# Optimization experiments

Hardware: AMD Instinct MI355X
Metric: run time of the kernel (lower is better)

## Reference

```python
import jax, jax.numpy as jnp
import numpy as np

N = 100000      # nodes
E = 1600000     # edges (avg degree 16)
IN_C = 128
OUT_C = 64
HID = 2 * OUT_C  # 128


def setup_inputs() -> dict:
    key = jax.random.key(0)
    ks = jax.random.split(key, 8)
    x = jax.random.normal(ks[0], (N, IN_C), dtype=jnp.float32)
    edge_index = jax.random.randint(ks[1], (2, E), 0, N, dtype=jnp.int32)
    # Glorot-ish init for GCN weight matrices, zero bias (PyG default)
    w1 = jax.random.normal(ks[2], (IN_C, HID), dtype=jnp.float32) / np.sqrt(IN_C)
    b1 = jnp.zeros((HID,), jnp.float32)
    w_mu = jax.random.normal(ks[3], (HID, OUT_C), dtype=jnp.float32) / np.sqrt(HID)
    b_mu = jnp.zeros((OUT_C,), jnp.float32)
    w_ls = jax.random.normal(ks[4], (HID, OUT_C), dtype=jnp.float32) / np.sqrt(HID)
    b_ls = jnp.zeros((OUT_C,), jnp.float32)
    return {"x": x, "edge_index": edge_index, "w1": w1, "b1": b1,
            "w_mu": w_mu, "b_mu": b_mu, "w_ls": w_ls, "b_ls": b_ls}


def _gcn_conv(h, w, b, src, dst, norm, n):
    # linear transform, then normalized sparse aggregation src -> dst
    h = h @ w                                   # [N, out]
    msg = h[src] * norm[:, None]                # [E+N, out] gather
    out = jax.ops.segment_sum(msg, dst, num_segments=n)  # scatter-add
    return out + b


def reference(x, edge_index, w1, b1, w_mu, b_mu, w_ls, b_ls):
    n = x.shape[0]
    # GCN normalization with self-loops (edge_weight=None -> all ones)
    loops = jnp.arange(n, dtype=edge_index.dtype)
    src = jnp.concatenate([edge_index[0], loops])
    dst = jnp.concatenate([edge_index[1], loops])
    ew = jnp.ones(src.shape[0], dtype=x.dtype)
    deg = jax.ops.segment_sum(ew, dst, num_segments=n)
    dinv = jnp.where(deg > 0, jax.lax.rsqrt(jnp.maximum(deg, 1e-12)), 0.0)
    norm = dinv[src] * ew * dinv[dst]           # D^-1/2 A_hat D^-1/2

    h = jax.nn.relu(_gcn_conv(x, w1, b1, src, dst, norm, n))
    mu = _gcn_conv(h, w_mu, b_mu, src, dst, norm, n)
    logstd = _gcn_conv(h, w_ls, b_ls, src, dst, norm, n)
    return (mu, logstd)
```

## Files before the change

kernel.cpp:

```cpp
#include <hip/hip_runtime.h>
#include <hip/hip_bf16.h>

#define CH 128
#define OC 64
#define NBINS 1024
#define NCHK  256
#define BSH   7

typedef __attribute__((ext_vector_type(4))) float f32x4;
typedef __attribute__((ext_vector_type(8))) float f32x8;
typedef __attribute__((ext_vector_type(8))) short bf16x8;
typedef __attribute__((ext_vector_type(8))) ushort u16x8;

static __device__ __forceinline__ float bf2f(ushort u) {
  return __uint_as_float(((unsigned)u) << 16);
}
static __device__ __forceinline__ ushort f2bf(float f) {
  __hip_bfloat16 h = __float2bfloat16(f);
  return *reinterpret_cast<ushort*>(&h);
}
static __device__ __forceinline__ void fma8(float w, u16x8 v, f32x8& a) {
#pragma unroll
  for (int j = 0; j < 8; j++) a[j] = fmaf(w, bf2f((ushort)v[j]), a[j]);
}

__global__ void k_pre(const float* __restrict__ x, ushort* __restrict__ y, int nx,
                      const float* __restrict__ w1, const float* __restrict__ wmu,
                      const float* __restrict__ wls, const float* __restrict__ bmu,
                      const float* __restrict__ bls, ushort* __restrict__ Wt0,
                      ushort* __restrict__ Wt1, float* __restrict__ bc) {
  int gid = blockIdx.x * 256 + threadIdx.x;
  int i = gid * 4;
  if (i < nx) {
    float4 v = *(const float4*)&x[i];
    ushort4 o; o.x = f2bf(v.x); o.y = f2bf(v.y); o.z = f2bf(v.z); o.w = f2bf(v.w);
    *(ushort4*)&y[i] = o;
  }
  if (gid < 16384) {
    int c = gid >> 7, k = gid & 127;
    Wt0[c * 128 + k] = f2bf(w1[k * 128 + c]);
    float v = (c < 64) ? wmu[k * 64 + c] : wls[k * 64 + (c - 64)];
    Wt1[c * 128 + k] = f2bf(v);
    if (gid < 128) bc[gid] = (gid < 64) ? bmu[gid] : bls[gid - 64];
  }
}


__global__ __launch_bounds__(256) void k_s1(const int* __restrict__ dst,
                                            int* __restrict__ bcnt, int ne, int cs) {
  __shared__ int h[NBINS];
  for (int j = threadIdx.x; j < NBINS; j += 256) h[j] = 0;
  __syncthreads();
  int e0 = blockIdx.x * cs, e1 = min(e0 + cs, ne);
  for (int e = e0 + threadIdx.x; e < e1; e += 256)
    atomicAdd(&h[dst[e] >> BSH], 1);
  __syncthreads();
  for (int j = threadIdx.x; j < NBINS; j += 256)
    bcnt[blockIdx.x * NBINS + j] = h[j];
}

__global__ __launch_bounds__(256) void k_s2a(const int* __restrict__ bcnt,
                                             int* __restrict__ curT,
                                             int* __restrict__ total) {
  __shared__ int s[NCHK];
  int b = blockIdx.x, t = threadIdx.x;
  int v = bcnt[t * NBINS + b];
  s[t] = v; __syncthreads();
  for (int off = 1; off < NCHK; off <<= 1) {
    int u = (t >= off) ? s[t - off] : 0;
    __syncthreads();
    s[t] += u;
    __syncthreads();
  }
  curT[b * NCHK + t] = s[t] - v;
  if (t == NCHK - 1) total[b] = s[t];
}

__global__ void k_s2b(const int* __restrict__ total, int* __restrict__ base) {
  __shared__ int s[256];
  int t = threadIdx.x;
  int loc[4]; int sum = 0;
#pragma unroll
  for (int j = 0; j < 4; j++) { loc[j] = total[t * 4 + j]; sum += loc[j]; }
  s[t] = sum; __syncthreads();
  int own = sum;
  for (int off = 1; off < 256; off <<= 1) {
    int u = (t >= off) ? s[t - off] : 0;
    __syncthreads();
    s[t] += u;
    __syncthreads();
  }
  int excl = s[t] - own;
#pragma unroll
  for (int j = 0; j < 4; j++) { base[t * 4 + j] = excl; excl += loc[j]; }
  if (t == 255) base[NBINS] = excl;
}

__global__ __launch_bounds__(256) void k_s3(const int* __restrict__ src,
    const int* __restrict__ dst, const int* __restrict__ curT,
    const int* __restrict__ base, unsigned* __restrict__ rec, int ne, int cs) {
  __shared__ int lcur[NBINS];
  int blk = blockIdx.x;
  for (int b = threadIdx.x; b < NBINS; b += 256)
    lcur[b] = curT[b * NCHK + blk] + base[b];
  __syncthreads();
  int e0 = blk * cs, e1 = min(e0 + cs, ne);
  for (int e = e0 + threadIdx.x; e < e1; e += 256) {
    int d = dst[e], sv = src[e];
    int pos = atomicAdd(&lcur[d >> BSH], 1);
    rec[pos] = ((unsigned)sv << BSH) | (unsigned)(d & 127);
  }
}

__global__ __launch_bounds__(256) void k_s4a(const unsigned* __restrict__ rec,
    const int* __restrict__ base, int* __restrict__ deg, int* __restrict__ rowptr,
    float* __restrict__ dinv, int nn) {
  __shared__ int h[128];
  __shared__ int sc[128];
  int b = blockIdx.x, tid = threadIdx.x;
  if (tid < 128) h[tid] = 0;
  __syncthreads();
  int r0 = base[b], r1 = base[b + 1];
  for (int r = r0 + tid; r < r1; r += 256)
    atomicAdd(&h[rec[r] & 127], 1);
  __syncthreads();
  if (tid < 128) sc[tid] = h[tid];
  __syncthreads();
  for (int off = 1; off < 128; off <<= 1) {
    int v = 0;
    if (tid < 128 && tid >= off) v = sc[tid - off];
    __syncthreads();
    if (tid < 128) sc[tid] += v;
    __syncthreads();
  }
  if (tid < 128) {
    int node = (b << BSH) + tid;
    if (node < nn) {
      int d = h[tid];
      deg[node] = d;
      rowptr[node] = r0 + sc[tid] - d;
      dinv[node] = rsqrtf((float)(d + 1));
    }
  }
}

__global__ __launch_bounds__(256) void k_s5(const unsigned* __restrict__ rec,
    const int* __restrict__ base, const int* __restrict__ rowptr,
    const int* __restrict__ deg, unsigned* __restrict__ csr, int nn) {
  __shared__ int lcur[128];
  int b = blockIdx.x, tid = threadIdx.x;
  if (tid < 128) {
    int node = (b << BSH) + tid;
    lcur[tid] = (node < nn) ? rowptr[node] : 0;
  }
  __syncthreads();
  int r0 = base[b], r1 = base[b + 1];
  for (int r = r0 + tid; r < r1; r += 256) {
    unsigned rc = rec[r];
    int s = (int)(rc >> BSH);
    int pos = atomicAdd(&lcur[rc & 127], 1);
    unsigned ds = (unsigned)min(deg[s], 32767);
    csr[pos] = (unsigned)s | (ds << 17);
  }
}

static __device__ __forceinline__ f32x8 gather_core(const ushort* __restrict__ in,
    const int* __restrict__ rowptr, const int* __restrict__ deg,
    const unsigned* __restrict__ csr, const float* __restrict__ dinv,
    int i, int lane16, float& di_out) {
  size_t loff = (size_t)lane16 * 8;
  int beg = rowptr[i];
  int cnt = deg[i];
  float di = dinv[i];
  u16x8 xv = *(const u16x8*)&in[(size_t)i * CH + loff];
  f32x8 acc = {0.f, 0.f, 0.f, 0.f, 0.f, 0.f, 0.f, 0.f};

  unsigned rec[8]; u16x8 row[4];
#pragma unroll
  for (int j = 0; j < 8; j++) rec[j] = (j < cnt) ? csr[beg + j] : 0u;
#pragma unroll
  for (int j = 0; j < 4; j++)
    if (j < cnt) row[j] = *(const u16x8*)&in[(size_t)(rec[j] & 0x1FFFFu) * CH + loff];

  int k = 0;
  while (cnt - k > 4) {
    unsigned nrec[4]; u16x8 nrow[4];
#pragma unroll
    for (int j = 0; j < 4; j++)
      nrec[j] = (k + 8 + j < cnt) ? csr[beg + k + 8 + j] : 0u;
#pragma unroll
    for (int j = 0; j < 4; j++)
      nrow[j] = (k + 4 + j < cnt)
              ? *(const u16x8*)&in[(size_t)(rec[4 + j] & 0x1FFFFu) * CH + loff]
              : row[j];
#pragma unroll
    for (int j = 0; j < 4; j++) {
      float w = rsqrtf((float)((rec[j] >> 17) + 1u));
      fma8(w, row[j], acc);
    }
#pragma unroll
    for (int j = 0; j < 4; j++) { rec[j] = rec[4 + j]; rec[4 + j] = nrec[j]; row[j] = nrow[j]; }
    k += 4;
  }
#pragma unroll
  for (int j = 0; j < 4; j++) {
    if (k + j < cnt) {
      float w = rsqrtf((float)((rec[j] >> 17) + 1u));
      fma8(w, row[j], acc);
    }
  }
  fma8(di, xv, acc);
  di_out = di;
  return acc;
}

__global__ __launch_bounds__(256) void k_aggemm(const ushort* __restrict__ in,
    const int* __restrict__ rowptr, const int* __restrict__ deg,
    const unsigned* __restrict__ csr, const float* __restrict__ dinv,
    const ushort* __restrict__ Wt0, const float* __restrict__ b1,
    const ushort* __restrict__ Wt1, ushort* __restrict__ P, int ntiles) {
  __shared__ ushort as_[16][136];
  __shared__ ushort hs[16][136];
  int tid = threadIdx.x;
  int node16 = tid >> 4, lane16 = tid & 15;
  int wv = tid >> 6;
  int lane = tid & 63;
  int l15 = lane & 15;
  int lk = (lane >> 4) * 8;
  bf16x8 bfrag1[2][4], bfrag2[2][4];
  float bias1[2];
#pragma unroll
  for (int ct = 0; ct < 2; ct++) {
    int bcol = wv * 32 + ct * 16 + l15;
#pragma unroll
    for (int kt = 0; kt < 4; kt++) {
      bfrag1[ct][kt] = *(const bf16x8*)&Wt0[(size_t)bcol * 128 + kt * 32 + lk];
      bfrag2[ct][kt] = *(const bf16x8*)&Wt1[(size_t)bcol * 128 + kt * 32 + lk];
    }
    bias1[ct] = b1[bcol];
  }
  for (int t = blockIdx.x; t < ntiles; t += gridDim.x) {
    int i = t * 16 + node16;
    float di;
    f32x8 acc = gather_core(in, rowptr, deg, csr, dinv, i, lane16, di);
    u16x8 o;
#pragma unroll
    for (int j = 0; j < 8; j++) o[j] = (short)f2bf(acc[j] * di);
    *(u16x8*)&as_[node16][lane16 * 8] = o;
    __syncthreads();
    bf16x8 af[4];
#pragma unroll
    for (int kt = 0; kt < 4; kt++) af[kt] = *(const bf16x8*)&as_[l15][kt * 32 + lk];
    f32x4 a1[2] = {{0.f, 0.f, 0.f, 0.f}, {0.f, 0.f, 0.f, 0.f}};
#pragma unroll
    for (int ct = 0; ct < 2; ct++)
#pragma unroll
      for (int kt = 0; kt < 4; kt++)
        a1[ct] = __builtin_amdgcn_mfma_f32_16x16x32_bf16(af[kt], bfrag1[ct][kt], a1[ct], 0, 0, 0);
#pragma unroll
    for (int ct = 0; ct < 2; ct++) {
      int col = wv * 32 + ct * 16 + l15;
#pragma unroll
      for (int r = 0; r < 4; r++)
        hs[(lane >> 4) * 4 + r][col] = f2bf(fmaxf(a1[ct][r] + bias1[ct], 0.f));
    }
    __syncthreads();
    bf16x8 af2[4];
#pragma unroll
    for (int kt = 0; kt < 4; kt++) af2[kt] = *(const bf16x8*)&hs[l15][kt * 32 + lk];
    f32x4 a2[2] = {{0.f, 0.f, 0.f, 0.f}, {0.f, 0.f, 0.f, 0.f}};
#pragma unroll
    for (int ct = 0; ct < 2; ct++)
#pragma unroll
      for (int kt = 0; kt < 4; kt++)
        a2[ct] = __builtin_amdgcn_mfma_f32_16x16x32_bf16(af2[kt], bfrag2[ct][kt], a2[ct], 0, 0, 0);
#pragma unroll
    for (int ct = 0; ct < 2; ct++) {
      int col = wv * 32 + ct * 16 + l15;
#pragma unroll
      for (int r = 0; r < 4; r++) {
        int node = t * 16 + (lane >> 4) * 4 + r;
        P[(size_t)node * CH + col] = f2bf(a2[ct][r]);
      }
    }
  }
}

__global__ __launch_bounds__(256) void k_aggout(const ushort* __restrict__ in,
                      float* __restrict__ oA, float* __restrict__ oB,
                      const float* __restrict__ bc,
                      const int* __restrict__ rowptr, const int* __restrict__ deg,
                      const unsigned* __restrict__ csr, const float* __restrict__ dinv,
                      int n) {
  int i = blockIdx.x * 16 + (threadIdx.x >> 4);
  if (i >= n) return;
  int lane = threadIdx.x & 15;
  float di;
  f32x8 acc = gather_core(in, rowptr, deg, csr, dinv, i, lane, di);
  f32x8 b8 = *(const f32x8*)&bc[lane * 8];
  f32x8 o;
#pragma unroll
  for (int j = 0; j < 8; j++) o[j] = acc[j] * di + b8[j];
  if (lane < 8) *(f32x8*)&oA[(size_t)i * OC + lane * 8] = o;
  else          *(f32x8*)&oB[(size_t)i * OC + (lane - 8) * 8] = o;
}


extern "C" void kernel_launch(void* const* d_in, const int* in_sizes, int n_in,
                              void* d_out, int out_size, void* d_ws, size_t ws_size,
                              hipStream_t stream) {
  const float* x   = (const float*)d_in[0];
  const int*   ei  = (const int*)d_in[1];
  const float* w1  = (const float*)d_in[2];
  const float* b1  = (const float*)d_in[3];
  const float* wmu = (const float*)d_in[4];
  const float* bmu = (const float*)d_in[5];
  const float* wls = (const float*)d_in[6];
  const float* bls = (const float*)d_in[7];
  float* out = (float*)d_out;

  const int nn = in_sizes[0] / CH;
  const int ne = in_sizes[1] / 2;
  const int* srcp = ei;
  const int* dstp = ei + ne;

  ushort*   B0   = (ushort*)d_ws;
  ushort*   B1   = B0 + (size_t)nn * CH;
  unsigned* csr  = (unsigned*)(B1 + (size_t)nn * CH);
  int*      deg  = (int*)(csr + ne);
  int*      rowptr = deg + nn;
  float*    dinv = (float*)(rowptr + nn);
  ushort*   Wt0  = (ushort*)(dinv + nn);
  ushort*   Wt1  = Wt0 + 128 * 128;
  float*    bc   = (float*)(Wt1 + 128 * 128);

  unsigned* rec  = (unsigned*)B1;
  int*      bcnt = (int*)(rec + ne);
  int*      curT = bcnt + NCHK * NBINS;
  int*      btot = curT + NBINS * NCHK;
  int*      bbase= btot + NBINS;

  const int NBUK = (nn + 127) >> BSH;
  const int cs = (ne + NCHK - 1) / NCHK;

  k_s1 <<<NCHK, 256, 0, stream>>>(dstp, bcnt, ne, cs);
  k_s2a<<<NBINS, NCHK, 0, stream>>>(bcnt, curT, btot);
  k_s2b<<<1, 256, 0, stream>>>(btot, bbase);
  k_s3 <<<NCHK, 256, 0, stream>>>(srcp, dstp, curT, bbase, rec, ne, cs);
  k_s4a<<<NBUK, 256, 0, stream>>>(rec, bbase, deg, rowptr, dinv, nn);
  k_s5 <<<NBUK, 256, 0, stream>>>(rec, bbase, rowptr, deg, csr, nn);
  k_pre<<<((nn * CH / 4) + 255) / 256, 256, 0, stream>>>(x, B0, nn * CH,
                                 w1, wmu, wls, bmu, bls, Wt0, Wt1, bc);

  const int ntiles = nn / 16;
  k_aggemm<<<2048, 256, 0, stream>>>(B0, rowptr, deg, csr, dinv,
                                     Wt0, b1, Wt1, B1, ntiles);
  k_aggout<<<(nn + 15) / 16, 256, 0, stream>>>(B1, out, out + (size_t)nn * OC, bc,
                                               rowptr, deg, csr, dinv, nn);
}
```

Before: 227.4 us.

## Split fused gather+GEMM into separate aggregation and GEMM kernels; transpose bin counts

Splits the first-layer aggregation out of the persistent gather+GEMM kernel into its own one-node-per-16-lanes kernel that writes the aggregated bf16 features to a buffer. A second kernel then reads that buffer straight into MFMA fragments for the two GEMMs, with a barrier added at the end of each tile. The goal is to remove the per-tile barrier stall that kept the irregular gather and the matrix work in lockstep, and to let the gather run at full occupancy. In exchange the aggregated features make an extra round trip through global memory. The histogram counts are also stored transposed so the scan kernel reads them coalesced.

```diff
diff --git a/kernel.cpp b/kernel.cpp
--- a/kernel.cpp
+++ b/kernel.cpp
@@ -47,7 +47,7 @@
 
 
 __global__ __launch_bounds__(256) void k_s1(const int* __restrict__ dst,
-                                            int* __restrict__ bcnt, int ne, int cs) {
+                                            int* __restrict__ bcntT, int ne, int cs) {
   __shared__ int h[NBINS];
   for (int j = threadIdx.x; j < NBINS; j += 256) h[j] = 0;
   __syncthreads();
@@ -56,15 +56,15 @@
     atomicAdd(&h[dst[e] >> BSH], 1);
   __syncthreads();
   for (int j = threadIdx.x; j < NBINS; j += 256)
-    bcnt[blockIdx.x * NBINS + j] = h[j];
-}
-
-__global__ __launch_bounds__(256) void k_s2a(const int* __restrict__ bcnt,
+    bcntT[j * NCHK + blockIdx.x] = h[j];
+}
+
+__global__ __launch_bounds__(256) void k_s2a(const int* __restrict__ bcntT,
                                              int* __restrict__ curT,
                                              int* __restrict__ total) {
   __shared__ int s[NCHK];
   int b = blockIdx.x, t = threadIdx.x;
-  int v = bcnt[t * NBINS + b];
+  int v = bcntT[b * NCHK + t];
   s[t] = v; __syncthreads();
   for (int off = 1; off < NCHK; off <<= 1) {
     int u = (t >= off) ? s[t - off] : 0;
@@ -214,24 +214,35 @@
   return acc;
 }
 
-__global__ __launch_bounds__(256) void k_aggemm(const ushort* __restrict__ in,
-    const int* __restrict__ rowptr, const int* __restrict__ deg,
-    const unsigned* __restrict__ csr, const float* __restrict__ dinv,
+__global__ __launch_bounds__(256) void k_agg0(const ushort* __restrict__ in,
+                      ushort* __restrict__ o16,
+                      const int* __restrict__ rowptr, const int* __restrict__ deg,
+                      const unsigned* __restrict__ csr, const float* __restrict__ dinv,
+                      int n) {
+  int i = blockIdx.x * 16 + (threadIdx.x >> 4);
+  if (i >= n) return;
+  int lane = threadIdx.x & 15;
+  float di;
+  f32x8 acc = gather_core(in, rowptr, deg, csr, dinv, i, lane, di);
+  u16x8 o;
+#pragma unroll
+  for (int j = 0; j < 8; j++) o[j] = (short)f2bf(acc[j] * di);
+  *(u16x8*)&o16[(size_t)i * CH + lane * 8] = o;
+}
+
+__global__ __launch_bounds__(256) void k_fused(const ushort* __restrict__ A,
     const ushort* __restrict__ Wt0, const float* __restrict__ b1,
     const ushort* __restrict__ Wt1, ushort* __restrict__ P, int ntiles) {
-  __shared__ ushort as_[16][136];
   __shared__ ushort hs[16][136];
-  int tid = threadIdx.x;
-  int node16 = tid >> 4, lane16 = tid & 15;
-  int wv = tid >> 6;
-  int lane = tid & 63;
+  int colg = threadIdx.x >> 6;
+  int lane = threadIdx.x & 63;
   int l15 = lane & 15;
   int lk = (lane >> 4) * 8;
   bf16x8 bfrag1[2][4], bfrag2[2][4];
   float bias1[2];
 #pragma unroll
   for (int ct = 0; ct < 2; ct++) {
-    int bcol = wv * 32 + ct * 16 + l15;
+    int bcol = colg * 32 + ct * 16 + l15;
 #pragma unroll
     for (int kt = 0; kt < 4; kt++) {
       bfrag1[ct][kt] = *(const bf16x8*)&Wt0[(size_t)bcol * 128 + kt * 32 + lk];
@@ -240,17 +251,10 @@
     bias1[ct] = b1[bcol];
   }
   for (int t = blockIdx.x; t < ntiles; t += gridDim.x) {
-    int i = t * 16 + node16;
-    float di;
-    f32x8 acc = gather_core(in, rowptr, deg, csr, dinv, i, lane16, di);
-    u16x8 o;
-#pragma unroll
-    for (int j = 0; j < 8; j++) o[j] = (short)f2bf(acc[j] * di);
-    *(u16x8*)&as_[node16][lane16 * 8] = o;
-    __syncthreads();
+    const ushort* ap = &A[(size_t)(t * 16 + l15) * CH + lk];
     bf16x8 af[4];
 #pragma unroll
-    for (int kt = 0; kt < 4; kt++) af[kt] = *(const bf16x8*)&as_[l15][kt * 32 + lk];
+    for (int kt = 0; kt < 4; kt++) af[kt] = *(const bf16x8*)&ap[kt * 32];
     f32x4 a1[2] = {{0.f, 0.f, 0.f, 0.f}, {0.f, 0.f, 0.f, 0.f}};
 #pragma unroll
     for (int ct = 0; ct < 2; ct++)
@@ -259,7 +263,7 @@
         a1[ct] = __builtin_amdgcn_mfma_f32_16x16x32_bf16(af[kt], bfrag1[ct][kt], a1[ct], 0, 0, 0);
 #pragma unroll
     for (int ct = 0; ct < 2; ct++) {
-      int col = wv * 32 + ct * 16 + l15;
+      int col = colg * 32 + ct * 16 + l15;
 #pragma unroll
       for (int r = 0; r < 4; r++)
         hs[(lane >> 4) * 4 + r][col] = f2bf(fmaxf(a1[ct][r] + bias1[ct], 0.f));
@@ -276,13 +280,14 @@
         a2[ct] = __builtin_amdgcn_mfma_f32_16x16x32_bf16(af2[kt], bfrag2[ct][kt], a2[ct], 0, 0, 0);
 #pragma unroll
     for (int ct = 0; ct < 2; ct++) {
-      int col = wv * 32 + ct * 16 + l15;
+      int col = colg * 32 + ct * 16 + l15;
 #pragma unroll
       for (int r = 0; r < 4; r++) {
         int node = t * 16 + (lane >> 4) * 4 + r;
         P[(size_t)node * CH + col] = f2bf(a2[ct][r]);
       }
     }
+    __syncthreads();
   }
 }
 
@@ -335,16 +340,16 @@
   float*    bc   = (float*)(Wt1 + 128 * 128);
 
   unsigned* rec  = (unsigned*)B1;
-  int*      bcnt = (int*)(rec + ne);
-  int*      curT = bcnt + NCHK * NBINS;
+  int*      bcntT= (int*)(rec + ne);
+  int*      curT = bcntT + NBINS * NCHK;
   int*      btot = curT + NBINS * NCHK;
   int*      bbase= btot + NBINS;
 
   const int NBUK = (nn + 127) >> BSH;
   const int cs = (ne + NCHK - 1) / NCHK;
 
-  k_s1 <<<NCHK, 256, 0, stream>>>(dstp, bcnt, ne, cs);
-  k_s2a<<<NBINS, NCHK, 0, stream>>>(bcnt, curT, btot);
+  k_s1 <<<NCHK, 256, 0, stream>>>(dstp, bcntT, ne, cs);
+  k_s2a<<<NBINS, NCHK, 0, stream>>>(bcntT, curT, btot);
   k_s2b<<<1, 256, 0, stream>>>(btot, bbase);
   k_s3 <<<NCHK, 256, 0, stream>>>(srcp, dstp, curT, bbase, rec, ne, cs);
   k_s4a<<<NBUK, 256, 0, stream>>>(rec, bbase, deg, rowptr, dinv, nn);
@@ -352,9 +357,11 @@
   k_pre<<<((nn * CH / 4) + 255) / 256, 256, 0, stream>>>(x, B0, nn * CH,
                                  w1, wmu, wls, bmu, bls, Wt0, Wt1, bc);
 
+  const int AB = (nn + 15) / 16;
   const int ntiles = nn / 16;
-  k_aggemm<<<2048, 256, 0, stream>>>(B0, rowptr, deg, csr, dinv,
-                                     Wt0, b1, Wt1, B1, ntiles);
-  k_aggout<<<(nn + 15) / 16, 256, 0, stream>>>(B1, out, out + (size_t)nn * OC, bc,
-                                               rowptr, deg, csr, dinv, nn);
-}
+
+  k_agg0<<<AB, 256, 0, stream>>>(B0, B1, rowptr, deg, csr, dinv, nn);
+  k_fused<<<1024, 256, 0, stream>>>(B1, Wt0, b1, Wt1, B0, ntiles);
+  k_aggout<<<AB, 256, 0, stream>>>(B0, out, out + (size_t)nn * OC, bc,
+                                   rowptr, deg, csr, dinv, nn);
+}
```

After: 215.7 us (median of 2 runs). 1.05x faster.
